# Optimization experiments

Hardware: AMD Instinct MI355X
Metric: run time of the kernel (lower is better)

The kernel has to match this reference:

```python
import jax, jax.numpy as jnp
import numpy as np

K = 3
PAD = 1
DG = 4
GN_GROUPS = 32
EPS = 1e-5


def deform_conv2d(x, offset, weight):
    # x: [B,C,H,W], offset: [B,DG*2*K*K,H,W] (mmcv layout: per group, per kernel tap, (dy,dx))
    B, C, H, W = x.shape
    KK = K * K
    cg = C // DG
    dt = x.dtype
    off = offset.reshape(B, DG, KK, 2, H, W)
    dy, dx = off[:, :, :, 0], off[:, :, :, 1]  # [B,DG,KK,H,W]
    ky, kx = jnp.meshgrid(jnp.arange(K), jnp.arange(K), indexing='ij')
    ky = ky.reshape(KK).astype(dt)
    kx = kx.reshape(KK).astype(dt)
    hh = jnp.arange(H, dtype=dt)
    ww = jnp.arange(W, dtype=dt)
    # sampling coords: p0 + p_k + offset (stride 1, dilation 1)
    y = hh[None, None, None, :, None] - PAD + ky[None, None, :, None, None] + dy
    xs = ww[None, None, None, None, :] - PAD + kx[None, None, :, None, None] + dx
    y0 = jnp.floor(y)
    x0 = jnp.floor(xs)
    wy1 = y - y0
    wx1 = xs - x0
    xg = x.reshape(B, DG, cg, H * W)

    def corner(yi, xi):
        # zero padding outside the feature map
        valid = (yi >= 0) & (yi < H) & (xi >= 0) & (xi < W)
        yc = jnp.clip(yi, 0, H - 1).astype(jnp.int32)
        xc = jnp.clip(xi, 0, W - 1).astype(jnp.int32)
        idx = (yc * W + xc).reshape(B, DG, KK * H * W)
        v = jax.vmap(jax.vmap(lambda xf, ix: xf[:, ix]))(xg, idx)  # [B,DG,cg,KK*H*W]
        v = v.reshape(B, DG, cg, KK, H, W)
        return v * valid.astype(dt)[:, :, None]

    col = (corner(y0, x0) * ((1 - wy1) * (1 - wx1))[:, :, None]
           + corner(y0, x0 + 1) * ((1 - wy1) * wx1)[:, :, None]
           + corner(y0 + 1, x0) * (wy1 * (1 - wx1))[:, :, None]
           + corner(y0 + 1, x0 + 1) * (wy1 * wx1)[:, :, None])  # [B,DG,cg,KK,H,W]
    col = col.reshape(B, C, KK, H, W)
    O = weight.shape[0]
    return jnp.einsum('ock,bckhw->bohw', weight.reshape(O, C, KK), col)


def group_norm(x, gamma, beta):
    B, C, H, W = x.shape
    xg = x.reshape(B, GN_GROUPS, -1)
    m = xg.mean(-1, keepdims=True)
    v = xg.var(-1, keepdims=True)
    xn = ((xg - m) * jax.lax.rsqrt(v + EPS)).reshape(B, C, H, W)
    return xn * gamma[None, :, None, None] + beta[None, :, None, None]


def setup_inputs() -> dict:
    key = jax.random.key(0)
    k1, k2, k3, k4 = jax.random.split(key, 4)
    B, C, H, W = 4, 256, 64, 64
    x = jax.random.normal(k1, (B, C, H, W), dtype=jnp.float32)
    shape = jax.random.normal(k2, (B, 4, H, W), dtype=jnp.float32)
    w_offset = jax.random.normal(k3, (DG * 2 * K * K, 4), dtype=jnp.float32) * 0.01
    w_deform = jax.random.normal(k4, (C, C, K, K), dtype=jnp.float32) * 0.01
    gamma = jnp.ones((C,), jnp.float32)
    beta = jnp.zeros((C,), jnp.float32)
    return {"x": x, "shape": shape, "w_offset": w_offset, "w_deform": w_deform, "gamma": gamma, "beta": beta}


def reference(x, shape, w_offset, w_deform, gamma, beta):
    # conv_offset: 1x1 conv on detached `shape`
    offset = jnp.einsum('oi,bihw->bohw', w_offset, jax.lax.stop_gradient(shape))
    out = deform_conv2d(x, offset, w_deform)
    return jax.nn.relu(group_norm(out, gamma, beta))
```

## Files before the change

kernel.cpp:

```cpp
#include <hip/hip_runtime.h>
#include <stdint.h>

#define BB   4
#define CCH  256
#define HH   64
#define WWD  64
#define HWSZ 4096
#define DGRP 4
#define CG   64
#define KKN  9
#define KT   2304
#define NND  16384
#define GNG  32
#define EPSV 1e-5f

#define WS_COLT  0
#define WS_WB    75497472
#define WS_G     76677120
#define WS_STATS 93454336
#define WS_PART  93455360

typedef __attribute__((ext_vector_type(8))) short short8;
typedef __attribute__((ext_vector_type(4))) float f32x4;

__device__ inline unsigned short f2bf(float f) {
    union { float f; unsigned u; } v; v.f = f;
    unsigned u = v.u;
    return (unsigned short)((u + 0x7FFFu + ((u >> 16) & 1u)) >> 16);
}

__device__ inline void gl_lds16(const void* g, void* l) {
    __builtin_amdgcn_global_load_lds(
        (const __attribute__((address_space(1))) void*)g,
        (__attribute__((address_space(3))) void*)l,
        16, 0, 0);
}

__global__ __launch_bounds__(256) void wconv_kernel(const float* __restrict__ wd,
                                                    unsigned short* __restrict__ Wb) {
    int idx = blockIdx.x * 256 + threadIdx.x;
    int o = idx / KT;
    int r = idx % KT;
    int kk = r >> 8;
    int c  = r & 255;
    Wb[idx] = f2bf(wd[o * KT + c * KKN + kk]);
}

__global__ __launch_bounds__(256) void col_kernel(const float* __restrict__ x,
                                                  const float* __restrict__ shp,
                                                  const float* __restrict__ woff,
                                                  unsigned short* __restrict__ colT) {
    __shared__ __align__(16) float xt[8 * 8 * 64 * 4];

    int bid   = blockIdx.x;
    int band  = bid & 15;
    int chalf = (bid >> 4) & 1;
    int dg    = (bid >> 5) & 3;
    int b     = bid >> 7;
    int h0    = band * 4;
    int tid   = threadIdx.x;
    int lane  = tid & 63;
    int wv    = tid >> 6;

    const float* xg = x + (size_t)(b * CCH + dg * CG + chalf * 32) * HWSZ;
    #pragma unroll 1
    for (int ii = 0; ii < 8; ++ii) {
        float v[8]; int la[8];
        #pragma unroll
        for (int u = 0; u < 8; ++u) {
            int idx = (ii * 8 + u) * 256 + tid;
            int w = idx & 63;
            int r = (idx >> 6) & 7;
            int j = idx >> 9;
            int gr = min(max(h0 - 2 + r, 0), HH - 1);
            v[u]  = xg[(size_t)j * HWSZ + gr * 64 + w];
            la[u] = ((j >> 2) * 8 + r) * 256 + w * 4 + (j & 3);
        }
        #pragma unroll
        for (int u = 0; u < 8; ++u) xt[la[u]] = v[u];
    }
    __syncthreads();

    int h  = h0 + wv;
    int hw = h * 64 + lane;
    float s0 = shp[(b * 4 + 0) * HWSZ + hw];
    float s1 = shp[(b * 4 + 1) * HWSZ + hw];
    float s2 = shp[(b * 4 + 2) * HWSZ + hw];
    float s3 = shp[(b * 4 + 3) * HWSZ + hw];

    unsigned short* rowp = colT + (size_t)(b * HWSZ + hw) * KT + dg * CG + chalf * 32;
    const char* xtb = (const char*)xt;

    #pragma unroll
    for (int kk = 0; kk < KKN; ++kk) {
        const float* wo = woff + (dg * 18 + kk * 2) * 4;
        float dy = wo[0] * s0 + wo[1] * s1 + wo[2] * s2 + wo[3] * s3;
        float dx = wo[4] * s0 + wo[5] * s1 + wo[6] * s2 + wo[7] * s3;

        int ky = kk / 3, kx = kk % 3;
        float y  = (float)(h - 1 + ky) + dy;
        float xs = (float)(lane - 1 + kx) + dx;
        float y0f = floorf(y), x0f = floorf(xs);
        float wy1 = y - y0f,  wx1 = xs - x0f;
        float wy0 = 1.f - wy1, wx0 = 1.f - wx1;
        int iy0 = (int)y0f, ix0 = (int)x0f;
        int iy1 = iy0 + 1,  ix1 = ix0 + 1;
        bool vy0 = (iy0 >= 0) && (iy0 < HH);
        bool vy1 = (iy1 >= 0) && (iy1 < HH);
        bool vx0 = (ix0 >= 0) && (ix0 < WWD);
        bool vx1 = (ix1 >= 0) && (ix1 < WWD);
        float w00 = (vy0 && vx0) ? wy0 * wx0 : 0.f;
        float w01 = (vy0 && vx1) ? wy0 * wx1 : 0.f;
        float w10 = (vy1 && vx0) ? wy1 * wx0 : 0.f;
        float w11 = (vy1 && vx1) ? wy1 * wx1 : 0.f;
        int cy0 = min(max(iy0, 0), HH - 1);
        int cy1 = min(max(iy1, 0), HH - 1);
        int cx0 = min(max(ix0, 0), WWD - 1);
        int cx1 = min(max(ix1, 0), WWD - 1);
        int ty0 = min(max(cy0 - (h0 - 2), 0), 7);
        int ty1 = min(max(cy1 - (h0 - 2), 0), 7);
        int a00 = (ty0 * 64 + cx0) * 16;
        int a01 = (ty0 * 64 + cx1) * 16;
        int a10 = (ty1 * 64 + cx0) * 16;
        int a11 = (ty1 * 64 + cx1) * 16;

        unsigned short tmp[32];
        #pragma unroll
        for (int c4g = 0; c4g < 8; ++c4g) {
            int base = c4g * 8192;
            const float4 v00 = *(const float4*)(xtb + base + a00);
            const float4 v01 = *(const float4*)(xtb + base + a01);
            const float4 v10 = *(const float4*)(xtb + base + a10);
            const float4 v11 = *(const float4*)(xtb + base + a11);
            float rx = w00 * v00.x + w01 * v01.x + w10 * v10.x + w11 * v11.x;
            float ry = w00 * v00.y + w01 * v01.y + w10 * v10.y + w11 * v11.y;
            float rz = w00 * v00.z + w01 * v01.z + w10 * v10.z + w11 * v11.z;
            float rw = w00 * v00.w + w01 * v01.w + w10 * v10.w + w11 * v11.w;
            tmp[c4g * 4 + 0] = f2bf(rx);
            tmp[c4g * 4 + 1] = f2bf(ry);
            tmp[c4g * 4 + 2] = f2bf(rz);
            tmp[c4g * 4 + 3] = f2bf(rw);
        }
        uint4* dst = (uint4*)(rowp + kk * 256);
        const uint4* src = (const uint4*)tmp;
        dst[0] = src[0];
        dst[1] = src[1];
        dst[2] = src[2];
        dst[3] = src[3];
    }
}

__global__ __launch_bounds__(256) void gemm_kernel(const unsigned short* __restrict__ Wb,
                                                   const unsigned short* __restrict__ colT,
                                                   float* __restrict__ G) {
    __shared__ __align__(16) short As[64 * 64];
    __shared__ __align__(16) short Bs[128 * 64];

    int tid  = threadIdx.x;
    int lane = tid & 63;
    int wv   = tid >> 6;
    int wm   = wv >> 1;
    int wn   = wv & 1;

    int idx  = blockIdx.x;
    int xcd  = idx & 7;
    int j2   = idx >> 3;
    int n0   = (xcd * 16 + (j2 >> 2)) * 128;
    int m0   = (j2 & 3) * 64;

    int r_a = tid >> 3;
    int s_a = tid & 7;
    int k_a = (s_a ^ (r_a & 7)) * 8;

    f32x4 acc[2][4] = {};

    int quad = lane >> 4;
    int lrow = lane & 15;
    int sw   = lrow & 7;

    for (int kt = 0; kt < KT; kt += 64) {
        #pragma unroll
        for (int u = 0; u < 2; ++u) {
            int rr = u * 32 + r_a;
            gl_lds16(Wb + (size_t)(m0 + rr) * KT + kt + k_a,
                     (short*)As + (u * 256 + tid) * 8);
        }
        #pragma unroll
        for (int u = 0; u < 4; ++u) {
            int rr = u * 32 + r_a;
            gl_lds16(colT + (size_t)(n0 + rr) * KT + kt + k_a,
                     (short*)Bs + (u * 256 + tid) * 8);
        }
        __syncthreads();

        #pragma unroll
        for (int kb = 0; kb < 2; ++kb) {
            int slot = (kb * 4 + quad) ^ sw;
            short8 a[2], b[4];
            #pragma unroll
            for (int i = 0; i < 2; ++i)
                a[i] = *(const short8*)&As[(wm * 32 + i * 16 + lrow) * 64 + slot * 8];
            #pragma unroll
            for (int j = 0; j < 4; ++j)
                b[j] = *(const short8*)&Bs[(wn * 64 + j * 16 + lrow) * 64 + slot * 8];
            #pragma unroll
            for (int i = 0; i < 2; ++i)
                #pragma unroll
                for (int j = 0; j < 4; ++j)
                    acc[i][j] = __builtin_amdgcn_mfma_f32_16x16x32_bf16(a[i], b[j], acc[i][j], 0, 0, 0);
        }
        __syncthreads();
    }

    #pragma unroll
    for (int i = 0; i < 2; ++i) {
        int m = m0 + wm * 32 + i * 16 + quad * 4;
        #pragma unroll
        for (int j = 0; j < 4; ++j) {
            int n = n0 + wn * 64 + j * 16 + lrow;
            #pragma unroll
            for (int r = 0; r < 4; ++r)
                G[(size_t)(m + r) * NND + n] = acc[i][j][r];
        }
    }
}

__global__ __launch_bounds__(256) void gn_part_kernel(const float* __restrict__ G,
                                                      float* __restrict__ partials) {
    int blk = blockIdx.x;
    int bg  = blk >> 3;
    int o   = blk & 7;
    int b   = bg >> 5;
    int g   = bg & 31;
    const float* row = G + (size_t)(g * 8 + o) * NND + b * HWSZ;
    float s1 = 0.f, s2 = 0.f;
    #pragma unroll
    for (int it = 0; it < 16; ++it) {
        float v = row[it * 256 + threadIdx.x];
        s1 += v;
        s2 += v * v;
    }
    #pragma unroll
    for (int off = 1; off < 64; off <<= 1) {
        s1 += __shfl_xor(s1, off);
        s2 += __shfl_xor(s2, off);
    }
    __shared__ float red[8];
    if ((threadIdx.x & 63) == 0) {
        red[(threadIdx.x >> 6) * 2]     = s1;
        red[(threadIdx.x >> 6) * 2 + 1] = s2;
    }
    __syncthreads();
    if (threadIdx.x == 0) {
        partials[blk * 2]     = red[0] + red[2] + red[4] + red[6];
        partials[blk * 2 + 1] = red[1] + red[3] + red[5] + red[7];
    }
}

__global__ __launch_bounds__(128) void gn_stats_kernel(const float* __restrict__ partials,
                                                       float* __restrict__ stats) {
    int bg = threadIdx.x;
    float t1 = 0.f, t2 = 0.f;
    #pragma unroll
    for (int o = 0; o < 8; ++o) {
        t1 += partials[(bg * 8 + o) * 2];
        t2 += partials[(bg * 8 + o) * 2 + 1];
    }
    const float invN = 1.f / 32768.f;
    float mean = t1 * invN;
    float var  = t2 * invN - mean * mean;
    stats[bg * 2]     = mean;
    stats[bg * 2 + 1] = rsqrtf(var + EPSV);
}

__global__ __launch_bounds__(256) void gn_apply_kernel(const float* __restrict__ G,
                                                       const float* __restrict__ stats,
                                                       const float* __restrict__ gamma,
                                                       const float* __restrict__ beta,
                                                       float* __restrict__ out) {
    int idx = blockIdx.x * 256 + threadIdx.x;
    int hw4 = idx & 1023;
    int o   = (idx >> 10) & 255;
    int b   = idx >> 18;
    int g   = o >> 3;
    float mean = stats[(b * 32 + g) * 2];
    float rstd = stats[(b * 32 + g) * 2 + 1];
    float ga = gamma[o], be = beta[o];
    const float4 v = *(const float4*)&G[(size_t)o * NND + b * HWSZ + hw4 * 4];
    float4 r;
    r.x = fmaxf(0.f, (v.x - mean) * rstd * ga + be);
    r.y = fmaxf(0.f, (v.y - mean) * rstd * ga + be);
    r.z = fmaxf(0.f, (v.z - mean) * rstd * ga + be);
    r.w = fmaxf(0.f, (v.w - mean) * rstd * ga + be);
    *(float4*)&out[(size_t)(b * CCH + o) * HWSZ + hw4 * 4] = r;
}

extern "C" void kernel_launch(void* const* d_in, const int* in_sizes, int n_in,
                              void* d_out, int out_size, void* d_ws, size_t ws_size,
                              hipStream_t stream) {
    const float* x     = (const float*)d_in[0];
    const float* shp   = (const float*)d_in[1];
    const float* woff  = (const float*)d_in[2];
    const float* wdef  = (const float*)d_in[3];
    const float* gamma = (const float*)d_in[4];
    const float* beta  = (const float*)d_in[5];
    float* out = (float*)d_out;

    char* ws = (char*)d_ws;
    unsigned short* colT = (unsigned short*)(ws + WS_COLT);
    unsigned short* Wb   = (unsigned short*)(ws + WS_WB);
    float* G             = (float*)(ws + WS_G);
    float* stats         = (float*)(ws + WS_STATS);
    float* partials      = (float*)(ws + WS_PART);

    wconv_kernel<<<2304, 256, 0, stream>>>(wdef, Wb);
    col_kernel<<<512, 256, 0, stream>>>(x, shp, woff, colT);
    gemm_kernel<<<512, 256, 0, stream>>>(Wb, colT, G);
    gn_part_kernel<<<1024, 256, 0, stream>>>(G, partials);
    gn_stats_kernel<<<1, 128, 0, stream>>>(partials, stats);
    gn_apply_kernel<<<4096, 256, 0, stream>>>(G, stats, gamma, beta, out);
}
```

Before: 151.9 us.

## Fuse GroupNorm statistics into GEMM epilogue and retile deformable column kernel

The GEMM epilogue now reduces per-group sum and sum-of-squares from its accumulators and atomically adds them into a zeroed partials buffer. This removes the separate partial-reduction and stats kernels and the extra full read of G, and the apply kernel computes mean and rstd inline. The column kernel is retiled to 8-row bands and 16-channel quarters, so each thread handles two rows with fewer channels, which changes halo overhead and per-thread register load. Float atomics make the statistics order-nondeterministic, and a memset is added to the launch sequence.

```diff
diff --git a/kernel.cpp b/kernel.cpp
--- a/kernel.cpp
+++ b/kernel.cpp
@@ -17,8 +17,7 @@
 #define WS_COLT  0
 #define WS_WB    75497472
 #define WS_G     76677120
-#define WS_STATS 93454336
-#define WS_PART  93455360
+#define WS_PART  93454336
 
 typedef __attribute__((ext_vector_type(8))) short short8;
 typedef __attribute__((ext_vector_type(4))) float f32x4;
@@ -50,111 +49,116 @@
                                                   const float* __restrict__ shp,
                                                   const float* __restrict__ woff,
                                                   unsigned short* __restrict__ colT) {
-    __shared__ __align__(16) float xt[8 * 8 * 64 * 4];
+    __shared__ __align__(16) float xt[4 * 12 * 64 * 4];
 
     int bid   = blockIdx.x;
-    int band  = bid & 15;
-    int chalf = (bid >> 4) & 1;
+    int band  = bid & 7;
+    int cq    = (bid >> 3) & 3;
     int dg    = (bid >> 5) & 3;
     int b     = bid >> 7;
-    int h0    = band * 4;
+    int h0    = band * 8;
     int tid   = threadIdx.x;
     int lane  = tid & 63;
     int wv    = tid >> 6;
 
-    const float* xg = x + (size_t)(b * CCH + dg * CG + chalf * 32) * HWSZ;
+    const float* xg = x + (size_t)(b * CCH + dg * CG + cq * 16) * HWSZ;
     #pragma unroll 1
-    for (int ii = 0; ii < 8; ++ii) {
+    for (int ii = 0; ii < 6; ++ii) {
         float v[8]; int la[8];
         #pragma unroll
         for (int u = 0; u < 8; ++u) {
             int idx = (ii * 8 + u) * 256 + tid;
-            int w = idx & 63;
-            int r = (idx >> 6) & 7;
-            int j = idx >> 9;
-            int gr = min(max(h0 - 2 + r, 0), HH - 1);
+            int j   = idx / 768;
+            int rem = idx - j * 768;
+            int r   = rem >> 6;
+            int w   = rem & 63;
+            int gr  = min(max(h0 - 2 + r, 0), HH - 1);
             v[u]  = xg[(size_t)j * HWSZ + gr * 64 + w];
-            la[u] = ((j >> 2) * 8 + r) * 256 + w * 4 + (j & 3);
+            la[u] = ((j >> 2) * 12 + r) * 256 + w * 4 + (j & 3);
         }
         #pragma unroll
         for (int u = 0; u < 8; ++u) xt[la[u]] = v[u];
     }
     __syncthreads();
 
-    int h  = h0 + wv;
-    int hw = h * 64 + lane;
-    float s0 = shp[(b * 4 + 0) * HWSZ + hw];
-    float s1 = shp[(b * 4 + 1) * HWSZ + hw];
-    float s2 = shp[(b * 4 + 2) * HWSZ + hw];
-    float s3 = shp[(b * 4 + 3) * HWSZ + hw];
-
-    unsigned short* rowp = colT + (size_t)(b * HWSZ + hw) * KT + dg * CG + chalf * 32;
     const char* xtb = (const char*)xt;
 
-    #pragma unroll
-    for (int kk = 0; kk < KKN; ++kk) {
-        const float* wo = woff + (dg * 18 + kk * 2) * 4;
-        float dy = wo[0] * s0 + wo[1] * s1 + wo[2] * s2 + wo[3] * s3;
-        float dx = wo[4] * s0 + wo[5] * s1 + wo[6] * s2 + wo[7] * s3;
-
-        int ky = kk / 3, kx = kk % 3;
-        float y  = (float)(h - 1 + ky) + dy;
-        float xs = (float)(lane - 1 + kx) + dx;
-        float y0f = floorf(y), x0f = floorf(xs);
-        float wy1 = y - y0f,  wx1 = xs - x0f;
-        float wy0 = 1.f - wy1, wx0 = 1.f - wx1;
-        int iy0 = (int)y0f, ix0 = (int)x0f;
-        int iy1 = iy0 + 1,  ix1 = ix0 + 1;
-        bool vy0 = (iy0 >= 0) && (iy0 < HH);
-        bool vy1 = (iy1 >= 0) && (iy1 < HH);
-        bool vx0 = (ix0 >= 0) && (ix0 < WWD);
-        bool vx1 = (ix1 >= 0) && (ix1 < WWD);
-        float w00 = (vy0 && vx0) ? wy0 * wx0 : 0.f;
-        float w01 = (vy0 && vx1) ? wy0 * wx1 : 0.f;
-        float w10 = (vy1 && vx0) ? wy1 * wx0 : 0.f;
-        float w11 = (vy1 && vx1) ? wy1 * wx1 : 0.f;
-        int cy0 = min(max(iy0, 0), HH - 1);
-        int cy1 = min(max(iy1, 0), HH - 1);
-        int cx0 = min(max(ix0, 0), WWD - 1);
-        int cx1 = min(max(ix1, 0), WWD - 1);
-        int ty0 = min(max(cy0 - (h0 - 2), 0), 7);
-        int ty1 = min(max(cy1 - (h0 - 2), 0), 7);
-        int a00 = (ty0 * 64 + cx0) * 16;
-        int a01 = (ty0 * 64 + cx1) * 16;
-        int a10 = (ty1 * 64 + cx0) * 16;
-        int a11 = (ty1 * 64 + cx1) * 16;
-
-        unsigned short tmp[32];
-        #pragma unroll
-        for (int c4g = 0; c4g < 8; ++c4g) {
-            int base = c4g * 8192;
-            const float4 v00 = *(const float4*)(xtb + base + a00);
-            const float4 v01 = *(const float4*)(xtb + base + a01);
-            const float4 v10 = *(const float4*)(xtb + base + a10);
-            const float4 v11 = *(const float4*)(xtb + base + a11);
-            float rx = w00 * v00.x + w01 * v01.x + w10 * v10.x + w11 * v11.x;
-            float ry = w00 * v00.y + w01 * v01.y + w10 * v10.y + w11 * v11.y;
-            float rz = w00 * v00.z + w01 * v01.z + w10 * v10.z + w11 * v11.z;
-            float rw = w00 * v00.w + w01 * v01.w + w10 * v10.w + w11 * v11.w;
-            tmp[c4g * 4 + 0] = f2bf(rx);
-            tmp[c4g * 4 + 1] = f2bf(ry);
-            tmp[c4g * 4 + 2] = f2bf(rz);
-            tmp[c4g * 4 + 3] = f2bf(rw);
-        }
-        uint4* dst = (uint4*)(rowp + kk * 256);
-        const uint4* src = (const uint4*)tmp;
-        dst[0] = src[0];
-        dst[1] = src[1];
-        dst[2] = src[2];
-        dst[3] = src[3];
+    #pragma unroll 1
+    for (int hr = 0; hr < 2; ++hr) {
+        int h  = h0 + wv * 2 + hr;
+        int hw = h * 64 + lane;
+        float s0 = shp[(b * 4 + 0) * HWSZ + hw];
+        float s1 = shp[(b * 4 + 1) * HWSZ + hw];
+        float s2 = shp[(b * 4 + 2) * HWSZ + hw];
+        float s3 = shp[(b * 4 + 3) * HWSZ + hw];
+
+        unsigned short* rowp = colT + (size_t)(b * HWSZ + hw) * KT + dg * CG + cq * 16;
+
+        #pragma unroll
+        for (int kk = 0; kk < KKN; ++kk) {
+            const float* wo = woff + (dg * 18 + kk * 2) * 4;
+            float dy = wo[0] * s0 + wo[1] * s1 + wo[2] * s2 + wo[3] * s3;
+            float dx = wo[4] * s0 + wo[5] * s1 + wo[6] * s2 + wo[7] * s3;
+
+            int ky = kk / 3, kx = kk % 3;
+            float y  = (float)(h - 1 + ky) + dy;
+            float xs = (float)(lane - 1 + kx) + dx;
+            float y0f = floorf(y), x0f = floorf(xs);
+            float wy1 = y - y0f,  wx1 = xs - x0f;
+            float wy0 = 1.f - wy1, wx0 = 1.f - wx1;
+            int iy0 = (int)y0f, ix0 = (int)x0f;
+            int iy1 = iy0 + 1,  ix1 = ix0 + 1;
+            bool vy0 = (iy0 >= 0) && (iy0 < HH);
+            bool vy1 = (iy1 >= 0) && (iy1 < HH);
+            bool vx0 = (ix0 >= 0) && (ix0 < WWD);
+            bool vx1 = (ix1 >= 0) && (ix1 < WWD);
+            float w00 = (vy0 && vx0) ? wy0 * wx0 : 0.f;
+            float w01 = (vy0 && vx1) ? wy0 * wx1 : 0.f;
+            float w10 = (vy1 && vx0) ? wy1 * wx0 : 0.f;
+            float w11 = (vy1 && vx1) ? wy1 * wx1 : 0.f;
+            int cy0 = min(max(iy0, 0), HH - 1);
+            int cy1 = min(max(iy1, 0), HH - 1);
+            int cx0 = min(max(ix0, 0), WWD - 1);
+            int cx1 = min(max(ix1, 0), WWD - 1);
+            int ty0 = min(max(cy0 - (h0 - 2), 0), 11);
+            int ty1 = min(max(cy1 - (h0 - 2), 0), 11);
+            int a00 = (ty0 * 64 + cx0) * 16;
+            int a01 = (ty0 * 64 + cx1) * 16;
+            int a10 = (ty1 * 64 + cx0) * 16;
+            int a11 = (ty1 * 64 + cx1) * 16;
+
+            unsigned short tmp[16];
+            #pragma unroll
+            for (int c4g = 0; c4g < 4; ++c4g) {
+                int base = c4g * 12288;
+                const float4 v00 = *(const float4*)(xtb + base + a00);
+                const float4 v01 = *(const float4*)(xtb + base + a01);
+                const float4 v10 = *(const float4*)(xtb + base + a10);
+                const float4 v11 = *(const float4*)(xtb + base + a11);
+                float rx = w00 * v00.x + w01 * v01.x + w10 * v10.x + w11 * v11.x;
+                float ry = w00 * v00.y + w01 * v01.y + w10 * v10.y + w11 * v11.y;
+                float rz = w00 * v00.z + w01 * v01.z + w10 * v10.z + w11 * v11.z;
+                float rw = w00 * v00.w + w01 * v01.w + w10 * v10.w + w11 * v11.w;
+                tmp[c4g * 4 + 0] = f2bf(rx);
+                tmp[c4g * 4 + 1] = f2bf(ry);
+                tmp[c4g * 4 + 2] = f2bf(rz);
+                tmp[c4g * 4 + 3] = f2bf(rw);
+            }
+            uint4* dst = (uint4*)(rowp + kk * 256);
+            const uint4* src = (const uint4*)tmp;
+            dst[0] = src[0];
+            dst[1] = src[1];
+        }
     }
 }
 
 __global__ __launch_bounds__(256) void gemm_kernel(const unsigned short* __restrict__ Wb,
                                                    const unsigned short* __restrict__ colT,
-                                                   float* __restrict__ G) {
+                                                   float* __restrict__ G,
+                                                   float* __restrict__ partials) {
     __shared__ __align__(16) short As[64 * 64];
     __shared__ __align__(16) short Bs[128 * 64];
+    __shared__ float sred[16];
 
     int tid  = threadIdx.x;
     int lane = tid & 63;
@@ -168,6 +172,8 @@
     int n0   = (xcd * 16 + (j2 >> 2)) * 128;
     int m0   = (j2 & 3) * 64;
 
+    if (tid < 16) sred[tid] = 0.f;
+
     int r_a = tid >> 3;
     int s_a = tid & 7;
     int k_a = (s_a ^ (r_a & 7)) * 8;
@@ -223,58 +229,40 @@
                 G[(size_t)(m + r) * NND + n] = acc[i][j][r];
         }
     }
-}
-
-__global__ __launch_bounds__(256) void gn_part_kernel(const float* __restrict__ G,
-                                                      float* __restrict__ partials) {
-    int blk = blockIdx.x;
-    int bg  = blk >> 3;
-    int o   = blk & 7;
-    int b   = bg >> 5;
-    int g   = bg & 31;
-    const float* row = G + (size_t)(g * 8 + o) * NND + b * HWSZ;
-    float s1 = 0.f, s2 = 0.f;
+
     #pragma unroll
-    for (int it = 0; it < 16; ++it) {
-        float v = row[it * 256 + threadIdx.x];
-        s1 += v;
-        s2 += v * v;
-    }
-    #pragma unroll
-    for (int off = 1; off < 64; off <<= 1) {
-        s1 += __shfl_xor(s1, off);
-        s2 += __shfl_xor(s2, off);
-    }
-    __shared__ float red[8];
-    if ((threadIdx.x & 63) == 0) {
-        red[(threadIdx.x >> 6) * 2]     = s1;
-        red[(threadIdx.x >> 6) * 2 + 1] = s2;
+    for (int i = 0; i < 2; ++i) {
+        float s1 = 0.f, s2 = 0.f;
+        #pragma unroll
+        for (int j = 0; j < 4; ++j)
+            #pragma unroll
+            for (int r = 0; r < 4; ++r) {
+                float v = acc[i][j][r];
+                s1 += v;
+                s2 += v * v;
+            }
+        #pragma unroll
+        for (int off = 1; off < 16; off <<= 1) {
+            s1 += __shfl_xor(s1, off);
+            s2 += __shfl_xor(s2, off);
+        }
+        if (lrow == 0) {
+            int gg = (wm * 32 + i * 16 + quad * 4) >> 3;
+            atomicAdd(&sred[gg * 2],     s1);
+            atomicAdd(&sred[gg * 2 + 1], s2);
+        }
     }
     __syncthreads();
-    if (threadIdx.x == 0) {
-        partials[blk * 2]     = red[0] + red[2] + red[4] + red[6];
-        partials[blk * 2 + 1] = red[1] + red[3] + red[5] + red[7];
-    }
-}
-
-__global__ __launch_bounds__(128) void gn_stats_kernel(const float* __restrict__ partials,
-                                                       float* __restrict__ stats) {
-    int bg = threadIdx.x;
-    float t1 = 0.f, t2 = 0.f;
-    #pragma unroll
-    for (int o = 0; o < 8; ++o) {
-        t1 += partials[(bg * 8 + o) * 2];
-        t2 += partials[(bg * 8 + o) * 2 + 1];
-    }
-    const float invN = 1.f / 32768.f;
-    float mean = t1 * invN;
-    float var  = t2 * invN - mean * mean;
-    stats[bg * 2]     = mean;
-    stats[bg * 2 + 1] = rsqrtf(var + EPSV);
+    if (tid < 8) {
+        int b  = n0 >> 12;
+        int g0 = m0 >> 3;
+        atomicAdd(&partials[(b * 32 + g0 + tid) * 2],     sred[tid * 2]);
+        atomicAdd(&partials[(b * 32 + g0 + tid) * 2 + 1], sred[tid * 2 + 1]);
+    }
 }
 
 __global__ __launch_bounds__(256) void gn_apply_kernel(const float* __restrict__ G,
-                                                       const float* __restrict__ stats,
+                                                       const float* __restrict__ partials,
                                                        const float* __restrict__ gamma,
                                                        const float* __restrict__ beta,
                                                        float* __restrict__ out) {
@@ -283,8 +271,12 @@
     int o   = (idx >> 10) & 255;
     int b   = idx >> 18;
     int g   = o >> 3;
-    float mean = stats[(b * 32 + g) * 2];
-    float rstd = stats[(b * 32 + g) * 2 + 1];
+    const float invN = 1.f / 32768.f;
+    float p1 = partials[(b * 32 + g) * 2];
+    float p2 = partials[(b * 32 + g) * 2 + 1];
+    float mean = p1 * invN;
+    float var  = p2 * invN - mean * mean;
+    float rstd = rsqrtf(var + EPSV);
     float ga = gamma[o], be = beta[o];
     const float4 v = *(const float4*)&G[(size_t)o * NND + b * HWSZ + hw4 * 4];
     float4 r;
@@ -310,13 +302,11 @@
     unsigned short* colT = (unsigned short*)(ws + WS_COLT);
     unsigned short* Wb   = (unsigned short*)(ws + WS_WB);
     float* G             = (float*)(ws + WS_G);
-    float* stats         = (float*)(ws + WS_STATS);
     float* partials      = (float*)(ws + WS_PART);
 
+    hipMemsetAsync(partials, 0, 128 * 2 * sizeof(float), stream);
     wconv_kernel<<<2304, 256, 0, stream>>>(wdef, Wb);
     col_kernel<<<512, 256, 0, stream>>>(x, shp, woff, colT);
-    gemm_kernel<<<512, 256, 0, stream>>>(Wb, colT, G);
-    gn_part_kernel<<<1024, 256, 0, stream>>>(G, partials);
-    gn_stats_kernel<<<1, 128, 0, stream>>>(partials, stats);
-    gn_apply_kernel<<<4096, 256, 0, stream>>>(G, stats, gamma, beta, out);
-}
+    gemm_kernel<<<512, 256, 0, stream>>>(Wb, colT, G, partials);
+    gn_apply_kernel<<<4096, 256, 0, stream>>>(G, partials, gamma, beta, out);
+}
```

After: 147.1 us. 3.1% less time.
